# Performance work log

Hardware: AMD Instinct MI355X
Metric: run time of the kernel (lower is better)

## Reference

```python
import jax, jax.numpy as jnp
import numpy as np

B, S, H, L, NH, DH, FF = 64, 256, 768, 12, 12, 64, 3072
V, MAXP, NTYPE, NI, NS = 30522, 512, 2, 10, 64


def setup_inputs() -> dict:
    key = jax.random.key(0)
    ks = iter(jax.random.split(key, 40))
    n = lambda shp, s=0.02: jax.random.normal(next(ks), shp, jnp.float32) * s
    inp = {
        'input_ids': jax.random.randint(next(ks), (B, S), 0, V),
        'attention_mask': jnp.ones((B, S), jnp.int32),
        'token_type_ids': jnp.zeros((B, S), jnp.int32),
        'intent_labels': jax.random.randint(next(ks), (B,), 0, NI),
        'slot_labels': jax.random.randint(next(ks), (B, S), 0, NS),
        'word_emb': n((V, H)), 'pos_emb': n((MAXP, H)), 'type_emb': n((NTYPE, H)),
        'emb_ln_g': jnp.ones((H,)), 'emb_ln_b': jnp.zeros((H,)),
        'Wq': n((L, H, H)), 'bq': jnp.zeros((L, H)),
        'Wk': n((L, H, H)), 'bk': jnp.zeros((L, H)),
        'Wv': n((L, H, H)), 'bv': jnp.zeros((L, H)),
        'Wo': n((L, H, H)), 'bo': jnp.zeros((L, H)),
        'ln1_g': jnp.ones((L, H)), 'ln1_b': jnp.zeros((L, H)),
        'W1': n((L, H, FF)), 'b1': jnp.zeros((L, FF)),
        'W2': n((L, FF, H)), 'b2': jnp.zeros((L, H)),
        'ln2_g': jnp.ones((L, H)), 'ln2_b': jnp.zeros((L, H)),
        'Wi': n((H, NI)), 'bi': jnp.zeros((NI,)),
        'Ws': n((H, NS)), 'bs': jnp.zeros((NS,)),
        'crf_start': n((NS,), 0.1), 'crf_end': n((NS,), 0.1),
        'crf_trans': n((NS, NS), 0.1),
    }
    return inp


def _ln(x, g, b):
    m = x.mean(-1, keepdims=True)
    v = jnp.square(x - m).mean(-1, keepdims=True)
    return (x - m) * jax.lax.rsqrt(v + 1e-12) * g + b


def _forward(params, input_ids, attention_mask, token_type_ids, intent_labels, slot_labels):
    (word_emb, pos_emb, type_emb, emb_ln_g, emb_ln_b,
     Wq, bq, Wk, bk, Wv, bv, Wo, bo, ln1_g, ln1_b,
     W1, b1, W2, b2, ln2_g, ln2_b,
     Wi, bi, Ws, bs, crf_start, crf_end, crf_trans) = params
    Bn, Sn = input_ids.shape
    Hn = word_emb.shape[1]
    dh = Hn // NH
    # BERT embeddings (dropout is identity in eval)
    x = word_emb[input_ids] + pos_emb[:Sn][None] + type_emb[token_type_ids]
    x = _ln(x, emb_ln_g, emb_ln_b)
    bias = (1.0 - attention_mask.astype(x.dtype))[:, None, None, :] * -1e9  # [B,1,1,S]

    def layer(h, p):
        wq, cq, wk, ck, wv, cv, wo, co, g1, d1, w1, e1, w2, e2, g2, d2 = p
        q = (h @ wq + cq).reshape(Bn, Sn, NH, dh)
        k = (h @ wk + ck).reshape(Bn, Sn, NH, dh)
        v = (h @ wv + cv).reshape(Bn, Sn, NH, dh)
        sc = jnp.einsum('bqnd,bknd->bnqk', q, k) / jnp.sqrt(jnp.float32(dh)) + bias
        a = jax.nn.softmax(sc, axis=-1)
        ctx = jnp.einsum('bnqk,bknd->bqnd', a, v).reshape(Bn, Sn, Hn)
        h2 = _ln(h + ctx @ wo + co, g1, d1)
        ff = jax.nn.gelu(h2 @ w1 + e1, approximate=False)
        return _ln(h2 + ff @ w2 + e2, g2, d2), None

    x, _ = jax.lax.scan(layer, x, (Wq, bq, Wk, bk, Wv, bv, Wo, bo,
                                   ln1_g, ln1_b, W1, b1, W2, b2, ln2_g, ln2_b))
    intent_logits = x[:, 0, :] @ Wi + bi           # [B, NI]
    slot_logits = x @ Ws + bs                      # [B, S, NS]
    # intent cross-entropy (mean over batch)
    lp = jax.nn.log_softmax(intent_logits, axis=-1)
    intent_loss = -jnp.take_along_axis(lp, intent_labels[:, None], axis=1).mean()
    # CRF log-likelihood
    mask = attention_mask.astype(slot_logits.dtype)
    em, tags = slot_logits, slot_labels
    t0 = tags[:, 0]
    score = crf_start[t0] + jnp.take_along_axis(em[:, 0, :], t0[:, None], axis=1)[:, 0]
    prev, cur = tags[:, :-1], tags[:, 1:]
    step_sc = crf_trans[prev, cur] + jnp.take_along_axis(em[:, 1:, :], cur[..., None], axis=2)[..., 0]
    score = score + (step_sc * mask[:, 1:]).sum(1)
    lengths = attention_mask.sum(1)
    last_tag = jnp.take_along_axis(tags, (lengths - 1)[:, None].astype(tags.dtype), axis=1)[:, 0]
    score = score + crf_end[last_tag]
    em_t = jnp.swapaxes(em, 0, 1)    # [S,B,C]
    mk_t = jnp.swapaxes(mask, 0, 1)  # [S,B]
    alpha0 = crf_start[None, :] + em_t[0]

    def crf_step(alpha, xs):
        e, m = xs
        nxt = jax.scipy.special.logsumexp(alpha[:, :, None] + crf_trans[None], axis=1) + e
        return jnp.where(m[:, None] > 0, nxt, alpha), None

    alpha, _ = jax.lax.scan(crf_step, alpha0, (em_t[1:], mk_t[1:]))
    logZ = jax.scipy.special.logsumexp(alpha + crf_end[None, :], axis=1)
    llh = score - logZ                # per-sequence log-likelihood
    crf_loss = -llh.mean()
    return intent_loss + 2.0 * crf_loss


def reference(input_ids, attention_mask, token_type_ids, intent_labels, slot_labels,
              word_emb, pos_emb, type_emb, emb_ln_g, emb_ln_b,
              Wq, bq, Wk, bk, Wv, bv, Wo, bo, ln1_g, ln1_b,
              W1, b1, W2, b2, ln2_g, ln2_b,
              Wi, bi, Ws, bs, crf_start, crf_end, crf_trans):
    params = (word_emb, pos_emb, type_emb, emb_ln_g, emb_ln_b,
              Wq, bq, Wk, bk, Wv, bv, Wo, bo, ln1_g, ln1_b,
              W1, b1, W2, b2, ln2_g, ln2_b,
              Wi, bi, Ws, bs, crf_start, crf_end, crf_trans)
    return _forward(params, input_ids, attention_mask, token_type_ids, intent_labels, slot_labels)
```

## Files before the change

kernel.cpp:

```cpp
#include <hip/hip_runtime.h>
#include <stdint.h>

typedef unsigned short u16;
typedef __attribute__((ext_vector_type(8))) short bh8;
typedef __attribute__((ext_vector_type(4))) float f4;

#define DEV static __device__ __forceinline__

DEV u16 f2bf(float f){ union{float f; uint32_t u;} v; v.f=f; uint32_t r=v.u + 0x7FFFu + ((v.u>>16)&1u); return (u16)(r>>16); }
DEV float bf2f(u16 u){ union{uint32_t u; float f;} v; v.u=((uint32_t)u)<<16; return v.f; }

DEV void mfma16(f4& d, bh8 a, bh8 b){
  asm("v_mfma_f32_16x16x32_bf16 %0, %1, %2, %0" : "+v"(d) : "v"(a), "v"(b));
}

#define FENCE16(A) asm volatile("s_nop 7\ns_nop 7" : \
 "+v"(A[0][0]),"+v"(A[0][1]),"+v"(A[0][2]),"+v"(A[0][3]),\
 "+v"(A[1][0]),"+v"(A[1][1]),"+v"(A[1][2]),"+v"(A[1][3]),\
 "+v"(A[2][0]),"+v"(A[2][1]),"+v"(A[2][2]),"+v"(A[2][3]),\
 "+v"(A[3][0]),"+v"(A[3][1]),"+v"(A[3][2]),"+v"(A[3][3]))

#define GLD16(g,l) __builtin_amdgcn_global_load_lds( \
    (__attribute__((address_space(1))) void*)(void*)(g), \
    (__attribute__((address_space(3))) void*)(void*)(l), 16, 0, 0)

struct GemmP { const u16* A; const u16* B; int K; void* C; int ldc;
               const float* b0; const float* b1; const float* b2; const u16* res; };

template<int EPI>
__global__ __launch_bounds__(256)
void gemm_bt(GemmP p){
  __shared__ __align__(16) u16 As[128*32];
  __shared__ __align__(16) u16 Bs[128*32];
  const int t=threadIdx.x, l=t&63, w=t>>6, wr=w>>1, wc=w&1;
  const int m0=blockIdx.x*128, n0=blockIdx.y*128;
  const u16* Ab = p.A + (size_t)m0*p.K;
  const u16* Bb = p.B + (size_t)n0*p.K;
  const int srow=l>>2, scol=(l&3)*8;
  f4 acc[4][4] = {};
  for(int k0=0;k0<p.K;k0+=32){
#pragma unroll
    for(int i=0;i<2;i++){
      const int c=w*2+i;
      GLD16(Ab + (size_t)(c*16+srow)*p.K + k0 + scol, &As[c*512]);
      GLD16(Bb + (size_t)(c*16+srow)*p.K + k0 + scol, &Bs[c*512]);
    }
    __syncthreads();
    bh8 af[4], bfr[4];
#pragma unroll
    for(int m=0;m<4;m++) af[m] = *(const bh8*)&As[(wr*64+m*16+(l&15))*32 + (l>>4)*8];
#pragma unroll
    for(int n=0;n<4;n++) bfr[n] = *(const bh8*)&Bs[(wc*64+n*16+(l&15))*32 + (l>>4)*8];
#pragma unroll
    for(int m=0;m<4;m++)
#pragma unroll
      for(int n=0;n<4;n++) mfma16(acc[m][n], af[m], bfr[n]);
    __syncthreads();
  }
  FENCE16(acc);
  const int lc=l&15, lr=(l>>4)*4;
#pragma unroll
  for(int m=0;m<4;m++)
#pragma unroll
  for(int n=0;n<4;n++)
#pragma unroll
  for(int r=0;r<4;r++){
    const int gr = m0 + wr*64 + m*16 + lr + r;
    const int gc = n0 + wc*64 + n*16 + lc;
    float v = acc[m][n][r];
    if(EPI==0){
      const float* bp = (gc<768)? p.b0 : (gc<1536? p.b1 : p.b2);
      const int bc = (gc<768)? gc : (gc<1536? gc-768 : gc-1536);
      ((u16*)p.C)[(size_t)gr*p.ldc + gc] = f2bf(v + bp[bc]);
    } else if(EPI==1){
      v += p.b0[gc] + bf2f(p.res[(size_t)gr*p.ldc + gc]);
      ((u16*)p.C)[(size_t)gr*p.ldc + gc] = f2bf(v);
    } else if(EPI==2){
      v += p.b0[gc];
      v = 0.5f*v*(1.f + erff(v*0.70710678118f));
      ((u16*)p.C)[(size_t)gr*p.ldc + gc] = f2bf(v);
    } else {
      v += (gc<64)? p.b0[gc] : 0.f;
      ((float*)p.C)[(size_t)gr*p.ldc + gc] = v;
    }
  }
}

__global__ __launch_bounds__(256)
void attn_kernel(const u16* __restrict__ qkv, const int* __restrict__ amask, u16* __restrict__ ctx){
  __shared__ __align__(16) u16 Ks[256*64];
  __shared__ __align__(16) u16 Vt[64*256];
  __shared__ __align__(16) u16 Ps[4*64*64];
  __shared__ float biasS[256];
  const int t=threadIdx.x, l=t&63, w=t>>6;
  const int b=blockIdx.x/12, h=blockIdx.x%12;
  biasS[t] = (1.f - (float)amask[b*256+t]) * -1e9f;
  const u16* kb = qkv + ((size_t)b*256)*2304 + 768 + h*64;
  const u16* vb = kb + 768;
#pragma unroll
  for(int i=0;i<8;i++){
    const int c = t + i*256;
    const int row = c>>3, seg = c&7;
    uint4 kv = *(const uint4*)(kb + (size_t)row*2304 + seg*8);
    const int ba = row*128 + seg*16;
    *(uint4*)((char*)Ks + (ba ^ ((row&7)<<4))) = kv;
    uint4 vv = *(const uint4*)(vb + (size_t)row*2304 + seg*8);
    const u16* pv = (const u16*)&vv;
#pragma unroll
    for(int j=0;j<8;j++){
      const int d = seg*8+j;
      const int bb = d*512 + row*2;
      *(u16*)((char*)Vt + (bb ^ ((d&7)<<4))) = pv[j];
    }
  }
  bh8 aq[4][2];
  const u16* qb = qkv + ((size_t)b*256 + w*64)*2304 + h*64;
#pragma unroll
  for(int m=0;m<4;m++)
#pragma unroll
    for(int ks=0;ks<2;ks++)
      aq[m][ks] = *(const bh8*)(qb + (size_t)(m*16+(l&15))*2304 + ks*32 + (l>>4)*8);
  __syncthreads();
  float mrun[4][4], lrun[4][4];
  f4 o[4][4] = {};
#pragma unroll
  for(int m=0;m<4;m++)
#pragma unroll
    for(int r=0;r<4;r++){ mrun[m][r] = -3e38f; lrun[m][r]=0.f; }
  u16* Pw = Ps + w*4096;
  for(int kt=0;kt<4;kt++){
    f4 sacc[4][4] = {};
#pragma unroll
    for(int ks=0;ks<2;ks++)
#pragma unroll
      for(int n=0;n<4;n++){
        const int row = kt*64 + n*16 + (l&15);
        const int by = row*128 + ks*64 + (l>>4)*16;
        bh8 bk = *(const bh8*)((const char*)Ks + (by ^ ((row&7)<<4)));
#pragma unroll
        for(int m=0;m<4;m++) mfma16(sacc[m][n], aq[m][ks], bk);
      }
    FENCE16(sacc);
#pragma unroll
    for(int m=0;m<4;m++){
      float rmax[4] = {-3e38f,-3e38f,-3e38f,-3e38f};
#pragma unroll
      for(int n=0;n<4;n++){
        const float bi = biasS[kt*64 + n*16 + (l&15)];
#pragma unroll
        for(int r=0;r<4;r++){
          float sv = sacc[m][n][r]*0.125f + bi;
          sacc[m][n][r] = sv;
          rmax[r] = fmaxf(rmax[r], sv);
        }
      }
#pragma unroll
      for(int dd=1; dd<16; dd<<=1)
#pragma unroll
        for(int r=0;r<4;r++) rmax[r] = fmaxf(rmax[r], __shfl_xor(rmax[r], dd));
      float psum[4];
#pragma unroll
      for(int r=0;r<4;r++){
        const float mn = fmaxf(mrun[m][r], rmax[r]);
        const float corr = __expf(mrun[m][r] - mn);
        mrun[m][r] = mn;
        lrun[m][r] *= corr;
#pragma unroll
        for(int nd=0; nd<4; nd++) o[m][nd][r] *= corr;
        psum[r] = 0.f;
      }
#pragma unroll
      for(int n=0;n<4;n++)
#pragma unroll
        for(int r=0;r<4;r++){
          const float pvv = __expf(sacc[m][n][r] - mrun[m][r]);
          sacc[m][n][r] = pvv;
          psum[r] += pvv;
        }
#pragma unroll
      for(int dd=1; dd<16; dd<<=1)
#pragma unroll
        for(int r=0;r<4;r++) psum[r] += __shfl_xor(psum[r], dd);
#pragma unroll
      for(int r=0;r<4;r++) lrun[m][r] += psum[r];
#pragma unroll
      for(int n=0;n<4;n++)
#pragma unroll
        for(int r=0;r<4;r++){
          const int prow = m*16 + (l>>4)*4 + r;
          const int pcol = n*16 + (l&15);
          const int by = prow*128 + pcol*2;
          *(u16*)((char*)Pw + (by ^ ((prow&7)<<4))) = f2bf(sacc[m][n][r]);
        }
    }
#pragma unroll
    for(int ks=0;ks<2;ks++){
      bh8 ap[4];
#pragma unroll
      for(int m=0;m<4;m++){
        const int prow = m*16 + (l&15);
        const int by = prow*128 + (ks*32 + (l>>4)*8)*2;
        ap[m] = *(const bh8*)((const char*)Pw + (by ^ ((prow&7)<<4)));
      }
#pragma unroll
      for(int nd=0; nd<4; nd++){
        const int dR = nd*16 + (l&15);
        const int by = dR*512 + (kt*64 + ks*32 + (l>>4)*8)*2;
        bh8 bv = *(const bh8*)((const char*)Vt + (by ^ ((dR&7)<<4)));
#pragma unroll
        for(int m=0;m<4;m++) mfma16(o[m][nd], ap[m], bv);
      }
    }
  }
  FENCE16(o);
#pragma unroll
  for(int m=0;m<4;m++)
#pragma unroll
  for(int nd=0; nd<4; nd++)
#pragma unroll
  for(int r=0;r<4;r++){
    const int row = w*64 + m*16 + (l>>4)*4 + r;
    const float vv = o[m][nd][r] / lrun[m][r];
    ctx[((size_t)b*256 + row)*768 + h*64 + nd*16 + (l&15)] = f2bf(vv);
  }
}

__global__ void ln_kernel(const u16* __restrict__ in, const float* __restrict__ g,
                          const float* __restrict__ b, u16* __restrict__ out){
  const int row = blockIdx.x, t = threadIdx.x;
  __shared__ float red[8];
  const u16* rp = in + (size_t)row*768;
  float v[3]; float s=0.f, q=0.f;
#pragma unroll
  for(int i=0;i<3;i++){ float x = bf2f(rp[t + i*256]); v[i]=x; s+=x; q+=x*x; }
#pragma unroll
  for(int dd=1; dd<64; dd<<=1){ s += __shfl_xor(s,dd); q += __shfl_xor(q,dd); }
  if((t&63)==0){ red[t>>6]=s; red[4+(t>>6)]=q; }
  __syncthreads();
  s = red[0]+red[1]+red[2]+red[3];
  q = red[4]+red[5]+red[6]+red[7];
  const float mean = s*(1.f/768.f);
  float var = q*(1.f/768.f) - mean*mean; var = fmaxf(var, 0.f);
  const float rs = rsqrtf(var + 1e-12f);
  u16* op = out + (size_t)row*768;
#pragma unroll
  for(int i=0;i<3;i++){ const int hh=t+i*256; op[hh] = f2bf((v[i]-mean)*rs*g[hh] + b[hh]); }
}

__global__ void embed_ln(const int* __restrict__ ids, const int* __restrict__ tti,
    const float* __restrict__ we, const float* __restrict__ pe, const float* __restrict__ te,
    const float* __restrict__ g, const float* __restrict__ bb, u16* __restrict__ x){
  const int tok = blockIdx.x, t = threadIdx.x;
  __shared__ float red[8];
  const int id = ids[tok], tyid = tti[tok], s0 = tok & 255;
  float v[3]; float s=0.f,q=0.f;
#pragma unroll
  for(int i=0;i<3;i++){
    const int hh = t+i*256;
    float x0 = we[(size_t)id*768+hh] + pe[(size_t)s0*768+hh] + te[(size_t)tyid*768+hh];
    v[i]=x0; s+=x0; q+=x0*x0;
  }
#pragma unroll
  for(int dd=1; dd<64; dd<<=1){ s += __shfl_xor(s,dd); q += __shfl_xor(q,dd); }
  if((t&63)==0){ red[t>>6]=s; red[4+(t>>6)]=q; }
  __syncthreads();
  s = red[0]+red[1]+red[2]+red[3];
  q = red[4]+red[5]+red[6]+red[7];
  const float mean = s*(1.f/768.f);
  float var = q*(1.f/768.f) - mean*mean; var = fmaxf(var, 0.f);
  const float rs = rsqrtf(var + 1e-12f);
#pragma unroll
  for(int i=0;i<3;i++){ const int hh=t+i*256; x[(size_t)tok*768+hh] = f2bf((v[i]-mean)*rs*g[hh] + bb[hh]); }
}

__global__ void transpose_cvt(const float* __restrict__ src, u16* __restrict__ dst, int R, int C){
  __shared__ float sm[32][33];
  const int ntc = C>>5;
  const int tr = blockIdx.x/ntc, tc = blockIdx.x - tr*ntc;
  const int r0 = tr<<5, c0 = tc<<5;
  const int tx = threadIdx.x, ty2 = threadIdx.y;
#pragma unroll
  for(int i=0;i<4;i++) sm[ty2+i*8][tx] = src[(size_t)(r0+ty2+i*8)*C + c0+tx];
  __syncthreads();
#pragma unroll
  for(int i=0;i<4;i++) dst[(size_t)(c0+ty2+i*8)*R + r0+tx] = f2bf(sm[tx][ty2+i*8]);
}

__global__ void conv_layer(const float* __restrict__ Wq, const float* __restrict__ Wk,
    const float* __restrict__ Wv, const float* __restrict__ Wo,
    const float* __restrict__ W1, const float* __restrict__ W2, u16* __restrict__ Wt){
  __shared__ float sm[32][33];
  const int bid = blockIdx.x;
  const float* src; u16* dst; int R, C, tt;
  if(bid<2304){
    R=768; C=768; const int mi = bid/576; tt = bid - mi*576;
    src = (mi==0?Wq: mi==1?Wk: mi==2?Wv: Wo);
    dst = Wt + (size_t)mi*589824;
  } else if(bid<4608){ R=768; C=3072; tt=bid-2304; src=W1; dst=Wt+2359296; }
  else { R=3072; C=768; tt=bid-4608; src=W2; dst=Wt+4718592; }
  const int ntc=C>>5; const int tr=tt/ntc, tc=tt-tr*ntc;
  const int r0=tr<<5, c0=tc<<5, tx=threadIdx.x, ty2=threadIdx.y;
#pragma unroll
  for(int i=0;i<4;i++) sm[ty2+i*8][tx] = src[(size_t)(r0+ty2+i*8)*C + c0+tx];
  __syncthreads();
#pragma unroll
  for(int i=0;i<4;i++) dst[(size_t)(c0+ty2+i*8)*R + r0+tx] = f2bf(sm[tx][ty2+i*8]);
}

__global__ void intent_kernel(const u16* __restrict__ x, const float* __restrict__ Wi,
    const float* __restrict__ bi, const int* __restrict__ lab, float* __restrict__ parts){
  const int b = blockIdx.x, t = threadIdx.x;
  __shared__ float xs[768];
  __shared__ float lg[10];
  const u16* rp = x + ((size_t)b*256)*768;
#pragma unroll
  for(int i=0;i<3;i++) xs[t+i*256] = bf2f(rp[t+i*256]);
  __syncthreads();
  if(t<10){
    float s = bi[t];
    for(int k=0;k<768;k++) s += xs[k]*Wi[(size_t)k*10 + t];
    lg[t] = s;
  }
  __syncthreads();
  if(t==0){
    float m = lg[0];
    for(int j=1;j<10;j++) m = fmaxf(m, lg[j]);
    float se = 0.f;
    for(int j=0;j<10;j++) se += expf(lg[j]-m);
    parts[b] = (logf(se) + m) - lg[lab[b]];
  }
}

__global__ __launch_bounds__(64)
void crf_kernel(const float* __restrict__ em, const int* __restrict__ tags,
    const int* __restrict__ amask, const float* __restrict__ cs, const float* __restrict__ ce,
    const float* __restrict__ tr, float* __restrict__ parts){
  const int b = blockIdx.x, j = threadIdx.x;
  const float* eb = em + (size_t)b*256*128;
  const int* tg = tags + b*256;
  const int* mk = amask + b*256;
  float Etr[64];
#pragma unroll
  for(int i=0;i<64;i++) Etr[i] = expf(tr[i*64 + j]);
  float sc = 0.f; int len = 0;
  for(int s=j+1; s<256; s+=64){
    const int pv = tg[s-1], cu = tg[s];
    sc += (tr[pv*64+cu] + eb[(size_t)s*128+cu]) * (float)mk[s];
  }
  for(int s=j; s<256; s+=64) len += mk[s];
#pragma unroll
  for(int dd=1; dd<64; dd<<=1){ sc += __shfl_xor(sc,dd); len += __shfl_xor(len,dd); }
  const int t0 = tg[0];
  float score = sc + cs[t0] + eb[t0] + ce[tg[len-1]];
  float alpha = cs[j] + eb[j];
  for(int s=1; s<256; s++){
    float am = alpha;
#pragma unroll
    for(int dd=1; dd<64; dd<<=1) am = fmaxf(am, __shfl_xor(am,dd));
    const float e = expf(alpha - am);
    float acc = 0.f;
#pragma unroll
    for(int i=0;i<64;i++) acc += __shfl(e, i) * Etr[i];
    const float nxt = logf(acc) + am + eb[(size_t)s*128 + j];
    alpha = (mk[s] > 0) ? nxt : alpha;
  }
  float v2 = alpha + ce[j];
  float am2 = v2;
#pragma unroll
  for(int dd=1; dd<64; dd<<=1) am2 = fmaxf(am2, __shfl_xor(am2,dd));
  float se = expf(v2 - am2);
#pragma unroll
  for(int dd=1; dd<64; dd<<=1) se += __shfl_xor(se,dd);
  if(j==0) parts[64+b] = (logf(se)+am2) - score;
}

__global__ void final_reduce(const float* __restrict__ parts, float* __restrict__ out){
  const int t = threadIdx.x;
  float a = parts[t], c = parts[64+t];
#pragma unroll
  for(int dd=1; dd<64; dd<<=1){ a += __shfl_xor(a,dd); c += __shfl_xor(c,dd); }
  if(t==0) out[0] = a*(1.f/64.f) + 2.f*c*(1.f/64.f);
}

extern "C" void kernel_launch(void* const* d_in, const int* in_sizes, int n_in,
                              void* d_out, int out_size, void* d_ws, size_t ws_size,
                              hipStream_t stream){
  (void)in_sizes; (void)n_in; (void)out_size;
  const int* ids   = (const int*)d_in[0];
  const int* amask = (const int*)d_in[1];
  const int* tti   = (const int*)d_in[2];
  const int* ilab  = (const int*)d_in[3];
  const int* slab  = (const int*)d_in[4];
  const float* we  = (const float*)d_in[5];
  const float* pe  = (const float*)d_in[6];
  const float* te  = (const float*)d_in[7];
  const float* eg  = (const float*)d_in[8];
  const float* ebt = (const float*)d_in[9];
  const float* Wq  = (const float*)d_in[10];
  const float* bq  = (const float*)d_in[11];
  const float* Wk  = (const float*)d_in[12];
  const float* bkk = (const float*)d_in[13];
  const float* Wv  = (const float*)d_in[14];
  const float* bvv = (const float*)d_in[15];
  const float* Wo  = (const float*)d_in[16];
  const float* bo  = (const float*)d_in[17];
  const float* l1g = (const float*)d_in[18];
  const float* l1b = (const float*)d_in[19];
  const float* W1  = (const float*)d_in[20];
  const float* b1  = (const float*)d_in[21];
  const float* W2  = (const float*)d_in[22];
  const float* b2  = (const float*)d_in[23];
  const float* l2g = (const float*)d_in[24];
  const float* l2b = (const float*)d_in[25];
  const float* Wi  = (const float*)d_in[26];
  const float* bi  = (const float*)d_in[27];
  const float* Wsp = (const float*)d_in[28];
  const float* bs  = (const float*)d_in[29];
  const float* cs  = (const float*)d_in[30];
  const float* ce  = (const float*)d_in[31];
  const float* ctr = (const float*)d_in[32];

  char* ws = (char*)d_ws;
  size_t off = 0;
  auto alloc = [&](size_t bytes)->void*{ void* p = ws + off; off += (bytes+255)&~(size_t)255; return p; };
  u16* x     = (u16*)alloc(16384ull*768*2);
  u16* h2    = (u16*)alloc(16384ull*768*2);
  u16* y     = (u16*)alloc(16384ull*768*2);
  u16* qkv   = (u16*)alloc(16384ull*2304*2);
  u16* cf    = (u16*)alloc(16384ull*3072*2);
  u16* Wt    = (u16*)alloc(7077888ull*2);
  u16* WsT   = (u16*)alloc(128ull*768*2);
  float* slots = (float*)alloc(16384ull*128*4);
  float* parts = (float*)alloc(512);
  if(off > ws_size) return;

  dim3 T256(256), T328(32,8);
  embed_ln<<<dim3(16384), T256, 0, stream>>>(ids, tti, we, pe, te, eg, ebt, x);
  transpose_cvt<<<dim3(48), T328, 0, stream>>>(Wsp, WsT, 768, 64);
  for(int L=0; L<12; L++){
    const size_t oH = (size_t)L*768*768, oF = (size_t)L*768*3072;
    conv_layer<<<dim3(6912), T328, 0, stream>>>(Wq+oH, Wk+oH, Wv+oH, Wo+oH, W1+oF, W2+oF, Wt);
    GemmP pq{ x, Wt, 768, qkv, 2304, bq+L*768, bkk+L*768, bvv+L*768, nullptr };
    gemm_bt<0><<<dim3(128,18), T256, 0, stream>>>(pq);
    attn_kernel<<<dim3(768), T256, 0, stream>>>(qkv, amask, cf);
    GemmP po{ cf, Wt+1769472, 768, y, 768, bo+L*768, nullptr, nullptr, x };
    gemm_bt<1><<<dim3(128,6), T256, 0, stream>>>(po);
    ln_kernel<<<dim3(16384), T256, 0, stream>>>(y, l1g+L*768, l1b+L*768, h2);
    GemmP p1{ h2, Wt+2359296, 768, cf, 3072, b1+L*3072, nullptr, nullptr, nullptr };
    gemm_bt<2><<<dim3(128,24), T256, 0, stream>>>(p1);
    GemmP p2{ cf, Wt+4718592, 3072, y, 768, b2+L*768, nullptr, nullptr, h2 };
    gemm_bt<1><<<dim3(128,6), T256, 0, stream>>>(p2);
    ln_kernel<<<dim3(16384), T256, 0, stream>>>(y, l2g+L*768, l2b+L*768, x);
  }
  GemmP psl{ x, WsT, 768, slots, 128, bs, nullptr, nullptr, nullptr };
  gemm_bt<3><<<dim3(128,1), T256, 0, stream>>>(psl);
  intent_kernel<<<dim3(64), T256, 0, stream>>>(x, Wi, bi, ilab, parts);
  crf_kernel<<<dim3(64), dim3(64), 0, stream>>>(slots, slab, amask, cs, ce, ctr, parts);
  final_reduce<<<dim3(1), dim3(64), 0, stream>>>(parts, (float*)d_out);
}
```

Baseline: 6.033 ms.

## Run CRF forward recursion in scaled linear space with LDS broadcast

Rewrites the CRF forward loop to work on exponentiated alpha values in linear space, renormalizing by lane 0's value every 8 steps and accumulating the log scale, instead of doing a max-reduce, exp and log every step. The 64-way broadcast now goes through shared memory with float4 reads rather than 64 shuffles, and next-step emission and mask loads are prefetched. The aim is to shorten the serial per-step latency of the 255-step recurrence. Fast-math exp/log and periodic-only rescaling add a risk of overflow or underflow if values drift by large factors within 8 steps, and the barrier pair adds some per-step synchronisation.

```diff
diff --git a/kernel.cpp b/kernel.cpp
--- a/kernel.cpp
+++ b/kernel.cpp
@@ -339,9 +339,10 @@
   const float* eb = em + (size_t)b*256*128;
   const int* tg = tags + b*256;
   const int* mk = amask + b*256;
+  __shared__ __align__(16) float aS[64];
   float Etr[64];
 #pragma unroll
-  for(int i=0;i<64;i++) Etr[i] = expf(tr[i*64 + j]);
+  for(int i=0;i<64;i++) Etr[i] = __expf(tr[i*64 + j]);
   float sc = 0.f; int len = 0;
   for(int s=j+1; s<256; s+=64){
     const int pv = tg[s-1], cu = tg[s];
@@ -352,23 +353,41 @@
   for(int dd=1; dd<64; dd<<=1){ sc += __shfl_xor(sc,dd); len += __shfl_xor(len,dd); }
   const int t0 = tg[0];
   float score = sc + cs[t0] + eb[t0] + ce[tg[len-1]];
-  float alpha = cs[j] + eb[j];
+  float a = __expf(cs[j] + eb[j]);
+  float logc = 0.f;
+  float em_s = eb[128 + j];
+  int   mk_s = mk[1];
   for(int s=1; s<256; s++){
-    float am = alpha;
-#pragma unroll
-    for(int dd=1; dd<64; dd<<=1) am = fmaxf(am, __shfl_xor(am,dd));
-    const float e = expf(alpha - am);
-    float acc = 0.f;
-#pragma unroll
-    for(int i=0;i<64;i++) acc += __shfl(e, i) * Etr[i];
-    const float nxt = logf(acc) + am + eb[(size_t)s*128 + j];
-    alpha = (mk[s] > 0) ? nxt : alpha;
-  }
-  float v2 = alpha + ce[j];
+    const int sn = (s<255)? s+1 : s;
+    const float em_n = eb[(size_t)sn*128 + j];
+    const int   mk_n = mk[sn];
+    aS[j] = a;
+    __syncthreads();
+    float acc0=0.f, acc1=0.f, acc2=0.f, acc3=0.f;
+    const float4* ap = (const float4*)aS;
+#pragma unroll
+    for(int q2=0;q2<16;q2++){
+      const float4 av = ap[q2];
+      acc0 += av.x*Etr[4*q2+0];
+      acc1 += av.y*Etr[4*q2+1];
+      acc2 += av.z*Etr[4*q2+2];
+      acc3 += av.w*Etr[4*q2+3];
+    }
+    __syncthreads();
+    const float nxt = ((acc0+acc1)+(acc2+acc3)) * __expf(em_s);
+    a = (mk_s > 0) ? nxt : a;
+    if((s&7)==7){
+      const float c = __shfl(a, 0);
+      logc += __logf(c);
+      a *= (1.f/c);
+    }
+    em_s = em_n; mk_s = mk_n;
+  }
+  float v2 = logf(a) + logc + ce[j];
   float am2 = v2;
 #pragma unroll
   for(int dd=1; dd<64; dd<<=1) am2 = fmaxf(am2, __shfl_xor(am2,dd));
-  float se = expf(v2 - am2);
+  float se = __expf(v2 - am2);
 #pragma unroll
   for(int dd=1; dd<64; dd<<=1) se += __shfl_xor(se,dd);
   if(j==0) parts[64+b] = (logf(se)+am2) - score;
```

New measurement: 5.481 ms. 9.1% less time.
